# Kernel optimization log

Measured on AMD Instinct MI355X. Metric: run time of the kernel, lower is better.

The kernel has to match this reference:

```python
import jax, jax.numpy as jnp
import numpy as np

N = 100000      # nodes
E = 1600000     # edges (avg degree 16)
D_IN, D_H1, D_H2, D_OUT = 512, 256, 256, 64


def setup_inputs() -> dict:
    key = jax.random.key(0)
    ks = jax.random.split(key, 8)
    x = jax.random.normal(ks[0], (N, D_IN), dtype=jnp.float32)
    row = jax.random.randint(ks[1], (E,), 0, N, dtype=jnp.int32)
    col = jax.random.randint(ks[2], (E,), 0, N, dtype=jnp.int32)
    vals = jax.random.uniform(ks[3], (E,), dtype=jnp.float32)
    # xavier-normal-ish scaling for weights
    W1 = jax.random.normal(ks[4], (D_IN, D_H1), dtype=jnp.float32) * np.sqrt(2.0 / (D_IN + D_H1))
    W2 = jax.random.normal(ks[5], (D_H1, D_H2), dtype=jnp.float32) * np.sqrt(2.0 / (D_H1 + D_H2))
    W3 = jax.random.normal(ks[6], (D_H2, D_OUT), dtype=jnp.float32) * np.sqrt(2.0 / (D_H2 + D_OUT))
    b1 = jnp.zeros((D_H1,), dtype=jnp.float32)
    b2 = jnp.zeros((D_H2,), dtype=jnp.float32)
    b3 = jnp.zeros((D_OUT,), dtype=jnp.float32)
    return {"x": x, "row": row, "col": col, "vals": vals,
            "W1": W1, "b1": b1, "W2": W2, "b2": b2, "W3": W3, "b3": b3}


def reference(x, row, col, vals, W1, b1, W2, b2, W3, b3):
    n = x.shape[0]

    def spmm(h):
        # out[i] = sum_{e: row[e]==i} vals[e] * h[col[e]]  (COO spmm)
        return jax.ops.segment_sum(vals[:, None] * h[col], row, num_segments=n)

    # layer 1: linear -> spmm -> relu  (dropout p=0 -> identity)
    h = jax.nn.relu(spmm(x @ W1 + b1))
    # layer 2
    h = jax.nn.relu(spmm(h @ W2 + b2))
    # output layer: no activation, no dropout
    return spmm(h @ W3 + b3)
```

## Files before the change

### kernel.cpp

```cpp
#include <hip/hip_runtime.h>

typedef _Float16 f16;
typedef _Float16 f16x4 __attribute__((ext_vector_type(4)));
typedef _Float16 f16x8 __attribute__((ext_vector_type(8)));
typedef float f32x4 __attribute__((ext_vector_type(4)));

#define DEVI __device__ __forceinline__

static constexpr int CAP = 64;

DEVI f16x8 cvt8(float4 a, float4 b) {
  f16x8 r;
  r[0] = (f16)a.x; r[1] = (f16)a.y; r[2] = (f16)a.z; r[3] = (f16)a.w;
  r[4] = (f16)b.x; r[5] = (f16)b.y; r[6] = (f16)b.z; r[7] = (f16)b.w;
  return r;
}

__global__ __launch_bounds__(256)
void prep_w(const float* __restrict__ W1, const float* __restrict__ W2,
            const float* __restrict__ W3, f16* __restrict__ WT1,
            f16* __restrict__ WT2, f16* __restrict__ WT3) {
  int t = blockIdx.x * 256 + threadIdx.x;
  const float* W; f16* O; int N; int u;
  if (t < 16384) {
    W = W1; O = WT1; N = 256; u = t;
  } else if (t < 16384 + 8192) {
    W = W2; O = WT2; N = 256; u = t - 16384;
  } else if (t < 16384 + 8192 + 2048) {
    W = W3; O = WT3; N = 64;  u = t - 24576;
  } else return;
  const int per = (N >> 4) * 64;
  const int kc = u / per;
  const int rem = u - kc * per;
  const int l = rem & 63;
  const int n = ((rem >> 6) << 4) + (l & 15);
  const int kb = kc * 32 + ((l >> 4) << 3);
  f16x8 o;
#pragma unroll
  for (int j = 0; j < 8; ++j) o[j] = (f16)W[(size_t)(kb + j) * N + n];
  *(f16x8*)(O + (size_t)u * 8) = o;
}

__global__ __launch_bounds__(256)
void build_slots(const int* __restrict__ row, const int* __restrict__ col,
                 const float* __restrict__ vals, int* __restrict__ cnt,
                 int2* __restrict__ slots, int E) {
  int e = blockIdx.x * 256 + threadIdx.x;
  if (e >= E) return;
  int r = row[e];
  int p = atomicAdd(&cnt[r], 1);
  if (p < CAP) slots[(size_t)r * CAP + p] = make_int2(col[e], __float_as_int(vals[e]));
}

__global__ __launch_bounds__(256, 2)
void gemm_l1_direct(const float* __restrict__ A, const f16* __restrict__ WT,
                    const float* __restrict__ bias, f16* __restrict__ C, int M) {
  constexpr int K = 512, N = 256;
  const int tid = threadIdx.x;
  const int wave = tid >> 6, lane = tid & 63;
  const int wm = wave >> 1, wn = wave & 1;
  const int quad = lane >> 4, l16 = lane & 15;
  const int r0 = blockIdx.x * 64 + wm * 32;

  const float4* ap0 = (const float4*)(A + (size_t)min(r0 + l16, M - 1) * K + quad * 8);
  const float4* ap1 = (const float4*)(A + (size_t)min(r0 + 16 + l16, M - 1) * K + quad * 8);
  const f16x8* bp = (const f16x8*)WT + (size_t)(wn * 8) * 64 + lane;

  f32x4 acc[2][8];
#pragma unroll
  for (int mt = 0; mt < 2; ++mt)
#pragma unroll
    for (int nt = 0; nt < 8; ++nt) {
      f32x4 z = {0.f, 0.f, 0.f, 0.f};
      acc[mt][nt] = z;
    }

  float4 ab[2][2][2];
  f16x8 bb[2][8];

#define L1_LOAD(P, KB)                                   \
  ab[P][0][0] = ap0[(KB) * 8];                           \
  ab[P][0][1] = ap0[(KB) * 8 + 1];                       \
  ab[P][1][0] = ap1[(KB) * 8];                           \
  ab[P][1][1] = ap1[(KB) * 8 + 1];                       \
  {                                                      \
    _Pragma("unroll")                                    \
    for (int nt = 0; nt < 8; ++nt)                       \
      bb[P][nt] = bp[((KB) * 16 + nt) * 64];             \
  }

  L1_LOAD(0, 0)
#pragma unroll
  for (int kb = 0; kb < 16; ++kb) {
    const int cur = kb & 1, nxt = cur ^ 1;
    if (kb + 1 < 16) { L1_LOAD(nxt, kb + 1) }
    f16x8 af0 = cvt8(ab[cur][0][0], ab[cur][0][1]);
    f16x8 af1 = cvt8(ab[cur][1][0], ab[cur][1][1]);
#pragma unroll
    for (int nt = 0; nt < 8; ++nt)
      acc[0][nt] = __builtin_amdgcn_mfma_f32_16x16x32_f16(af0, bb[cur][nt], acc[0][nt], 0, 0, 0);
#pragma unroll
    for (int nt = 0; nt < 8; ++nt)
      acc[1][nt] = __builtin_amdgcn_mfma_f32_16x16x32_f16(af1, bb[cur][nt], acc[1][nt], 0, 0, 0);
  }
#undef L1_LOAD

  float bv[8];
#pragma unroll
  for (int nt = 0; nt < 8; ++nt) bv[nt] = bias[wn * 128 + nt * 16 + l16];
#pragma unroll
  for (int mt = 0; mt < 2; ++mt) {
#pragma unroll
    for (int nt = 0; nt < 8; ++nt) {
      int colg = wn * 128 + nt * 16 + l16;
#pragma unroll
      for (int r = 0; r < 4; ++r) {
        int grow = r0 + mt * 16 + quad * 4 + r;
        if (grow < M)
          C[(size_t)grow * N + colg] = (f16)(acc[mt][nt][r] + bv[nt]);
      }
    }
  }
}

template <int NTILES>
__global__ __launch_bounds__(256, 2)
void gemm_direct(const f16* __restrict__ A, const f16* __restrict__ WT,
                 const float* __restrict__ bias, f16* __restrict__ C, int M) {
  constexpr int K = 256, N = NTILES * 64, NF16 = N / 16;
  const int tid = threadIdx.x;
  const int wave = tid >> 6, lane = tid & 63;
  const int quad = lane >> 4, l16 = lane & 15;
  const int gw = blockIdx.x * 4 + wave;
  const int mtile = (NTILES == 1) ? gw : (gw / NTILES);
  const int ntile = (NTILES == 1) ? 0 : (gw % NTILES);
  const int r0 = mtile * 64;
  if (r0 >= M) return;

  const f16x8* ap0 = (const f16x8*)(A + (size_t)min(r0 + l16, M - 1) * K) + quad;
  const f16x8* ap1 = (const f16x8*)(A + (size_t)min(r0 + 16 + l16, M - 1) * K) + quad;
  const f16x8* ap2 = (const f16x8*)(A + (size_t)min(r0 + 32 + l16, M - 1) * K) + quad;
  const f16x8* ap3 = (const f16x8*)(A + (size_t)min(r0 + 48 + l16, M - 1) * K) + quad;
  const f16x8* bp = (const f16x8*)WT + (size_t)(ntile * 4) * 64 + lane;

  f32x4 acc[4][4];
#pragma unroll
  for (int mt = 0; mt < 4; ++mt)
#pragma unroll
    for (int nt = 0; nt < 4; ++nt) {
      f32x4 z = {0.f, 0.f, 0.f, 0.f};
      acc[mt][nt] = z;
    }

  f16x8 ab[2][4], bb[2][4];

#define GD_LOAD(P, KB)                                   \
  ab[P][0] = ap0[(KB) * 4];                              \
  ab[P][1] = ap1[(KB) * 4];                              \
  ab[P][2] = ap2[(KB) * 4];                              \
  ab[P][3] = ap3[(KB) * 4];                              \
  {                                                      \
    _Pragma("unroll")                                    \
    for (int nt = 0; nt < 4; ++nt)                       \
      bb[P][nt] = bp[((KB) * NF16 + nt) * 64];           \
  }

  GD_LOAD(0, 0)
#pragma unroll
  for (int kb = 0; kb < 8; ++kb) {
    const int cur = kb & 1, nxt = cur ^ 1;
    if (kb + 1 < 8) { GD_LOAD(nxt, kb + 1) }
#pragma unroll
    for (int mt = 0; mt < 4; ++mt)
#pragma unroll
      for (int nt = 0; nt < 4; ++nt)
        acc[mt][nt] = __builtin_amdgcn_mfma_f32_16x16x32_f16(ab[cur][mt], bb[cur][nt], acc[mt][nt], 0, 0, 0);
  }
#undef GD_LOAD

  float bv[4];
#pragma unroll
  for (int nt = 0; nt < 4; ++nt) bv[nt] = bias[ntile * 64 + nt * 16 + l16];
#pragma unroll
  for (int mt = 0; mt < 4; ++mt) {
#pragma unroll
    for (int nt = 0; nt < 4; ++nt) {
      int colg = ntile * 64 + nt * 16 + l16;
#pragma unroll
      for (int r = 0; r < 4; ++r) {
        int grow = r0 + mt * 16 + quad * 4 + r;
        if (grow < M)
          C[(size_t)grow * N + colg] = (f16)(acc[mt][nt][r] + bv[nt]);
      }
    }
  }
}

__global__ __launch_bounds__(256)
void spmm_relu256(const f16* __restrict__ T, const int2* __restrict__ slots,
                  const int* __restrict__ cnt, f16* __restrict__ H, int nrows) {
  const int wave = threadIdx.x >> 6, lane = threadIdx.x & 63;
  const int i = blockIdx.x * 4 + wave;
  if (i >= nrows) return;
  const int c = min(cnt[i], CAP);
  const int2* sl = slots + (size_t)i * CAP;
  float a0 = 0.f, a1 = 0.f, a2 = 0.f, a3 = 0.f;
  int j = 0;
  for (; j + 8 <= c; j += 8) {
    int2 e[8];
#pragma unroll
    for (int q = 0; q < 8; ++q) e[q] = sl[j + q];
    f16x4 u[8];
#pragma unroll
    for (int q = 0; q < 8; ++q)
      u[q] = ((const f16x4*)(T + (size_t)e[q].x * 256))[lane];
#pragma unroll
    for (int q = 0; q < 8; ++q) {
      float v = __int_as_float(e[q].y);
      a0 += v * (float)u[q].x; a1 += v * (float)u[q].y;
      a2 += v * (float)u[q].z; a3 += v * (float)u[q].w;
    }
  }
  for (; j + 2 <= c; j += 2) {
    int2 e0 = sl[j], e1 = sl[j + 1];
    f16x4 u0 = ((const f16x4*)(T + (size_t)e0.x * 256))[lane];
    f16x4 u1 = ((const f16x4*)(T + (size_t)e1.x * 256))[lane];
    float v0 = __int_as_float(e0.y), v1 = __int_as_float(e1.y);
    a0 += v0 * (float)u0.x + v1 * (float)u1.x;
    a1 += v0 * (float)u0.y + v1 * (float)u1.y;
    a2 += v0 * (float)u0.z + v1 * (float)u1.z;
    a3 += v0 * (float)u0.w + v1 * (float)u1.w;
  }
  if (j < c) {
    int2 e = sl[j];
    f16x4 u = ((const f16x4*)(T + (size_t)e.x * 256))[lane];
    float v = __int_as_float(e.y);
    a0 += v * (float)u.x; a1 += v * (float)u.y;
    a2 += v * (float)u.z; a3 += v * (float)u.w;
  }
  f16x4 o;
  o.x = (f16)fmaxf(a0, 0.f); o.y = (f16)fmaxf(a1, 0.f);
  o.z = (f16)fmaxf(a2, 0.f); o.w = (f16)fmaxf(a3, 0.f);
  ((f16x4*)(H + (size_t)i * 256))[lane] = o;
}

__global__ __launch_bounds__(256)
void spmm_out64(const f16* __restrict__ T, const int2* __restrict__ slots,
                const int* __restrict__ cnt, float* __restrict__ out, int nrows) {
  const int wave = threadIdx.x >> 6, lane = threadIdx.x & 63;
  const int i = blockIdx.x * 4 + wave;
  if (i >= nrows) return;
  const int c = min(cnt[i], CAP);
  const int2* sl = slots + (size_t)i * CAP;
  float a = 0.f;
  int j = 0;
  for (; j + 8 <= c; j += 8) {
    int2 e[8];
#pragma unroll
    for (int q = 0; q < 8; ++q) e[q] = sl[j + q];
    float u[8];
#pragma unroll
    for (int q = 0; q < 8; ++q) u[q] = (float)T[(size_t)e[q].x * 64 + lane];
#pragma unroll
    for (int q = 0; q < 8; ++q) a += __int_as_float(e[q].y) * u[q];
  }
  for (; j < c; ++j) {
    int2 e = sl[j];
    a += __int_as_float(e.y) * (float)T[(size_t)e.x * 64 + lane];
  }
  out[(size_t)i * 64 + lane] = a;
}

extern "C" void kernel_launch(void* const* d_in, const int* in_sizes, int n_in,
                              void* d_out, int out_size, void* d_ws, size_t ws_size,
                              hipStream_t stream) {
  const float* x    = (const float*)d_in[0];
  const int*   row  = (const int*)d_in[1];
  const int*   col  = (const int*)d_in[2];
  const float* vals = (const float*)d_in[3];
  const float* W1   = (const float*)d_in[4];
  const float* b1   = (const float*)d_in[5];
  const float* W2   = (const float*)d_in[6];
  const float* b2   = (const float*)d_in[7];
  const float* W3   = (const float*)d_in[8];
  const float* b3   = (const float*)d_in[9];
  float* out = (float*)d_out;

  const int N = in_sizes[0] / 512;
  const int E = in_sizes[1];

  char* ws = (char*)d_ws;
  const size_t MiB = 1ull << 20;
  int*  cnt   = (int*)ws;
  int2* slots = (int2*)(ws + 1 * MiB);
  f16*  WT1   = (f16*)(ws + 52 * MiB);
  f16*  WT2   = WT1 + 256 * 512;
  f16*  WT3   = WT2 + 256 * 256;
  f16*  T     = (f16*)(ws + 53 * MiB);
  f16*  H     = (f16*)(ws + 104 * MiB);

  hipMemsetAsync(cnt, 0, (size_t)N * sizeof(int), stream);
  prep_w<<<(16384 + 8192 + 2048 + 255) / 256, 256, 0, stream>>>(W1, W2, W3, WT1, WT2, WT3);
  build_slots<<<(E + 255) / 256, 256, 0, stream>>>(row, col, vals, cnt, slots, E);

  const int mt64 = (N + 63) / 64;
  dim3 gs((N + 3) / 4);

  gemm_l1_direct<<<mt64, 256, 0, stream>>>(x, WT1, b1, T, N);
  spmm_relu256<<<gs, 256, 0, stream>>>(T, slots, cnt, H, N);
  gemm_direct<4><<<mt64, 256, 0, stream>>>(H, WT2, b2, T, N);
  spmm_relu256<<<gs, 256, 0, stream>>>(T, slots, cnt, H, N);
  gemm_direct<1><<<(mt64 + 3) / 4, 256, 0, stream>>>(H, WT3, b3, T, N);
  spmm_out64<<<gs, 256, 0, stream>>>(T, slots, cnt, out, N);
}
```

Measured before the change: 845.5 us.

## Stage GEMM tiles through LDS with async global-to-LDS triple buffering

After: 836.0 us. No clear change (-1.1%).

```diff
diff --git a/kernel.cpp b/kernel.cpp
--- a/kernel.cpp
+++ b/kernel.cpp
@@ -8,6 +8,16 @@
 #define DEVI __device__ __forceinline__
 
 static constexpr int CAP = 64;
+
+#define WAITVM(N) asm volatile("s_waitcnt vmcnt(" #N ")" ::: "memory")
+#define WAITLGKM0 asm volatile("s_waitcnt lgkmcnt(0)" ::: "memory")
+#define BAR() __builtin_amdgcn_s_barrier()
+
+DEVI void g2l16(const void* g, void* l) {
+  __builtin_amdgcn_global_load_lds(
+      (const __attribute__((address_space(1))) void*)g,
+      (__attribute__((address_space(3))) void*)l, 16, 0, 0);
+}
 
 DEVI f16x8 cvt8(float4 a, float4 b) {
   f16x8 r;
@@ -52,96 +62,23 @@
   if (p < CAP) slots[(size_t)r * CAP + p] = make_int2(col[e], __float_as_int(vals[e]));
 }
 
-__global__ __launch_bounds__(256, 2)
-void gemm_l1_direct(const float* __restrict__ A, const f16* __restrict__ WT,
-                    const float* __restrict__ bias, f16* __restrict__ C, int M) {
-  constexpr int K = 512, N = 256;
+__global__ __launch_bounds__(256)
+void gemm_l1_pipe(const float* __restrict__ A, const f16* __restrict__ WT,
+                  const float* __restrict__ bias, f16* __restrict__ C, int M) {
+  constexpr int NK = 16;
+  __shared__ f16 As[2][128 * 32];
+  __shared__ f16 Bs[3][128 * 32];
+
   const int tid = threadIdx.x;
   const int wave = tid >> 6, lane = tid & 63;
   const int wm = wave >> 1, wn = wave & 1;
   const int quad = lane >> 4, l16 = lane & 15;
-  const int r0 = blockIdx.x * 64 + wm * 32;
-
-  const float4* ap0 = (const float4*)(A + (size_t)min(r0 + l16, M - 1) * K + quad * 8);
-  const float4* ap1 = (const float4*)(A + (size_t)min(r0 + 16 + l16, M - 1) * K + quad * 8);
-  const f16x8* bp = (const f16x8*)WT + (size_t)(wn * 8) * 64 + lane;
-
-  f32x4 acc[2][8];
-#pragma unroll
-  for (int mt = 0; mt < 2; ++mt)
-#pragma unroll
-    for (int nt = 0; nt < 8; ++nt) {
-      f32x4 z = {0.f, 0.f, 0.f, 0.f};
-      acc[mt][nt] = z;
-    }
-
-  float4 ab[2][2][2];
-  f16x8 bb[2][8];
-
-#define L1_LOAD(P, KB)                                   \
-  ab[P][0][0] = ap0[(KB) * 8];                           \
-  ab[P][0][1] = ap0[(KB) * 8 + 1];                       \
-  ab[P][1][0] = ap1[(KB) * 8];                           \
-  ab[P][1][1] = ap1[(KB) * 8 + 1];                       \
-  {                                                      \
-    _Pragma("unroll")                                    \
-    for (int nt = 0; nt < 8; ++nt)                       \
-      bb[P][nt] = bp[((KB) * 16 + nt) * 64];             \
-  }
-
-  L1_LOAD(0, 0)
-#pragma unroll
-  for (int kb = 0; kb < 16; ++kb) {
-    const int cur = kb & 1, nxt = cur ^ 1;
-    if (kb + 1 < 16) { L1_LOAD(nxt, kb + 1) }
-    f16x8 af0 = cvt8(ab[cur][0][0], ab[cur][0][1]);
-    f16x8 af1 = cvt8(ab[cur][1][0], ab[cur][1][1]);
-#pragma unroll
-    for (int nt = 0; nt < 8; ++nt)
-      acc[0][nt] = __builtin_amdgcn_mfma_f32_16x16x32_f16(af0, bb[cur][nt], acc[0][nt], 0, 0, 0);
-#pragma unroll
-    for (int nt = 0; nt < 8; ++nt)
-      acc[1][nt] = __builtin_amdgcn_mfma_f32_16x16x32_f16(af1, bb[cur][nt], acc[1][nt], 0, 0, 0);
-  }
-#undef L1_LOAD
-
-  float bv[8];
-#pragma unroll
-  for (int nt = 0; nt < 8; ++nt) bv[nt] = bias[wn * 128 + nt * 16 + l16];
-#pragma unroll
-  for (int mt = 0; mt < 2; ++mt) {
-#pragma unroll
-    for (int nt = 0; nt < 8; ++nt) {
-      int colg = wn * 128 + nt * 16 + l16;
-#pragma unroll
-      for (int r = 0; r < 4; ++r) {
-        int grow = r0 + mt * 16 + quad * 4 + r;
-        if (grow < M)
-          C[(size_t)grow * N + colg] = (f16)(acc[mt][nt][r] + bv[nt]);
-      }
-    }
-  }
-}
-
-template <int NTILES>
-__global__ __launch_bounds__(256, 2)
-void gemm_direct(const f16* __restrict__ A, const f16* __restrict__ WT,
-                 const float* __restrict__ bias, f16* __restrict__ C, int M) {
-  constexpr int K = 256, N = NTILES * 64, NF16 = N / 16;
-  const int tid = threadIdx.x;
-  const int wave = tid >> 6, lane = tid & 63;
-  const int quad = lane >> 4, l16 = lane & 15;
-  const int gw = blockIdx.x * 4 + wave;
-  const int mtile = (NTILES == 1) ? gw : (gw / NTILES);
-  const int ntile = (NTILES == 1) ? 0 : (gw % NTILES);
-  const int r0 = mtile * 64;
-  if (r0 >= M) return;
-
-  const f16x8* ap0 = (const f16x8*)(A + (size_t)min(r0 + l16, M - 1) * K) + quad;
-  const f16x8* ap1 = (const f16x8*)(A + (size_t)min(r0 + 16 + l16, M - 1) * K) + quad;
-  const f16x8* ap2 = (const f16x8*)(A + (size_t)min(r0 + 32 + l16, M - 1) * K) + quad;
-  const f16x8* ap3 = (const f16x8*)(A + (size_t)min(r0 + 48 + l16, M - 1) * K) + quad;
-  const f16x8* bp = (const f16x8*)WT + (size_t)(ntile * 4) * 64 + lane;
+  const int r0 = blockIdx.x * 128;
+  const int bn = blockIdx.y;
+
+  const float* asrc0 = A + (size_t)min(r0 + (wave * 2 + 0) * 16 + l16, M - 1) * 512 + quad * 8;
+  const float* asrc1 = A + (size_t)min(r0 + (wave * 2 + 1) * 16 + l16, M - 1) * 512 + quad * 8;
+  const f16* bsrc = WT + ((size_t)(bn * 8 + wave * 2)) * 512 + lane * 8;
 
   f32x4 acc[4][4];
 #pragma unroll
@@ -152,45 +89,153 @@
       acc[mt][nt] = z;
     }
 
-  f16x8 ab[2][4], bb[2][4];
-
-#define GD_LOAD(P, KB)                                   \
-  ab[P][0] = ap0[(KB) * 4];                              \
-  ab[P][1] = ap1[(KB) * 4];                              \
-  ab[P][2] = ap2[(KB) * 4];                              \
-  ab[P][3] = ap3[(KB) * 4];                              \
-  {                                                      \
-    _Pragma("unroll")                                    \
-    for (int nt = 0; nt < 4; ++nt)                       \
-      bb[P][nt] = bp[((KB) * NF16 + nt) * 64];           \
-  }
-
-  GD_LOAD(0, 0)
-#pragma unroll
-  for (int kb = 0; kb < 8; ++kb) {
-    const int cur = kb & 1, nxt = cur ^ 1;
-    if (kb + 1 < 8) { GD_LOAD(nxt, kb + 1) }
+  float4 ra[2][2][2];
+
+#define P1_ISSUE(KB, SET, BS)                                          \
+  {                                                                    \
+    const float4* pa0 = (const float4*)(asrc0 + (KB) * 32);            \
+    ra[SET][0][0] = pa0[0]; ra[SET][0][1] = pa0[1];                    \
+    const float4* pa1 = (const float4*)(asrc1 + (KB) * 32);            \
+    ra[SET][1][0] = pa1[0]; ra[SET][1][1] = pa1[1];                    \
+    g2l16(bsrc + (size_t)(KB) * 16 * 512, &Bs[BS][(wave * 2) * 512]);  \
+    g2l16(bsrc + (size_t)(KB) * 16 * 512 + 512,                        \
+          &Bs[BS][(wave * 2 + 1) * 512]);                              \
+  }
+#define P1_CVT(SET, SL)                                                \
+  *(f16x8*)&As[SL][(wave * 2) * 512 + lane * 8] =                      \
+      cvt8(ra[SET][0][0], ra[SET][0][1]);                              \
+  *(f16x8*)&As[SL][(wave * 2 + 1) * 512 + lane * 8] =                  \
+      cvt8(ra[SET][1][0], ra[SET][1][1]);
+
+  P1_ISSUE(0, 0, 0)
+  P1_ISSUE(1, 1, 1)
+  WAITVM(8);
+  P1_CVT(0, 0)
+
+#pragma unroll
+  for (int kb = 0; kb < NK; ++kb) {
+    if (kb < NK - 2) { P1_ISSUE(kb + 2, kb & 1, (kb + 2) % 3) }
+    if (kb < NK - 2) { WAITVM(8); }
+    else if (kb == NK - 2) { WAITVM(2); }
+    else { WAITVM(0); }
+    if (kb < NK - 1) { P1_CVT((kb + 1) & 1, (kb + 1) & 1) }
+    WAITLGKM0;
+    BAR();
+    f16x8 af[4], bf[4];
 #pragma unroll
     for (int mt = 0; mt < 4; ++mt)
+      af[mt] = *(const f16x8*)&As[kb & 1][(wm * 4 + mt) * 512 + lane * 8];
+#pragma unroll
+    for (int nt = 0; nt < 4; ++nt)
+      bf[nt] = *(const f16x8*)&Bs[kb % 3][(wn * 4 + nt) * 512 + lane * 8];
+#pragma unroll
+    for (int mt = 0; mt < 4; ++mt)
 #pragma unroll
       for (int nt = 0; nt < 4; ++nt)
-        acc[mt][nt] = __builtin_amdgcn_mfma_f32_16x16x32_f16(ab[cur][mt], bb[cur][nt], acc[mt][nt], 0, 0, 0);
-  }
-#undef GD_LOAD
+        acc[mt][nt] = __builtin_amdgcn_mfma_f32_16x16x32_f16(af[mt], bf[nt], acc[mt][nt], 0, 0, 0);
+    BAR();
+  }
+#undef P1_ISSUE
+#undef P1_CVT
 
   float bv[4];
 #pragma unroll
-  for (int nt = 0; nt < 4; ++nt) bv[nt] = bias[ntile * 64 + nt * 16 + l16];
+  for (int nt = 0; nt < 4; ++nt) bv[nt] = bias[bn * 128 + wn * 64 + nt * 16 + l16];
 #pragma unroll
   for (int mt = 0; mt < 4; ++mt) {
 #pragma unroll
     for (int nt = 0; nt < 4; ++nt) {
-      int colg = ntile * 64 + nt * 16 + l16;
+      int colg = bn * 128 + wn * 64 + nt * 16 + l16;
 #pragma unroll
       for (int r = 0; r < 4; ++r) {
-        int grow = r0 + mt * 16 + quad * 4 + r;
+        int grow = r0 + wm * 64 + mt * 16 + quad * 4 + r;
         if (grow < M)
-          C[(size_t)grow * N + colg] = (f16)(acc[mt][nt][r] + bv[nt]);
+          C[(size_t)grow * 256 + colg] = (f16)(acc[mt][nt][r] + bv[nt]);
+      }
+    }
+  }
+}
+
+template <int BN, int NTOT>
+__global__ __launch_bounds__(256)
+void gemm_pipe(const f16* __restrict__ A, const f16* __restrict__ WT,
+               const float* __restrict__ bias, f16* __restrict__ C, int M) {
+  constexpr int NT = BN / 32, BFRAGS = BN / 16, NB = BN / 64;
+  constexpr int NF16 = NTOT / 16, NK = 8;
+  __shared__ f16 As[3][128 * 32];
+  __shared__ f16 Bs[3][BN * 32];
+
+  const int tid = threadIdx.x;
+  const int wave = tid >> 6, lane = tid & 63;
+  const int wm = wave >> 1, wn = wave & 1;
+  const int quad = lane >> 4, l16 = lane & 15;
+  const int r0 = blockIdx.x * 128;
+  const int bn = blockIdx.y;
+
+  const f16* asrc0 = A + (size_t)min(r0 + (wave * 2 + 0) * 16 + l16, M - 1) * 256 + quad * 8;
+  const f16* asrc1 = A + (size_t)min(r0 + (wave * 2 + 1) * 16 + l16, M - 1) * 256 + quad * 8;
+  const f16* bsrc = WT + (size_t)(bn * BFRAGS + wave * NB) * 512 + lane * 8;
+
+  f32x4 acc[4][NT];
+#pragma unroll
+  for (int mt = 0; mt < 4; ++mt)
+#pragma unroll
+    for (int nt = 0; nt < NT; ++nt) {
+      f32x4 z = {0.f, 0.f, 0.f, 0.f};
+      acc[mt][nt] = z;
+    }
+
+#define P2_ISSUE(KB, SL)                                               \
+  {                                                                    \
+    g2l16(asrc0 + (KB) * 32, &As[SL][(wave * 2) * 512]);               \
+    g2l16(asrc1 + (KB) * 32, &As[SL][(wave * 2 + 1) * 512]);           \
+    _Pragma("unroll")                                                  \
+    for (int t = 0; t < NB; ++t)                                       \
+      g2l16(bsrc + ((size_t)(KB) * NF16 + t) * 512,                    \
+            &Bs[SL][(wave * NB + t) * 512]);                           \
+  }
+
+  P2_ISSUE(0, 0)
+  P2_ISSUE(1, 1)
+
+#pragma unroll
+  for (int kb = 0; kb < NK; ++kb) {
+    if (kb < NK - 2) { P2_ISSUE(kb + 2, (kb + 2) % 3) }
+    if (kb < NK - 2) {
+      if constexpr (BN == 128) { WAITVM(8); } else { WAITVM(6); }
+    } else if (kb == NK - 2) {
+      if constexpr (BN == 128) { WAITVM(4); } else { WAITVM(3); }
+    } else { WAITVM(0); }
+    BAR();
+    f16x8 af[4], bf[NT];
+#pragma unroll
+    for (int mt = 0; mt < 4; ++mt)
+      af[mt] = *(const f16x8*)&As[kb % 3][(wm * 4 + mt) * 512 + lane * 8];
+#pragma unroll
+    for (int nt = 0; nt < NT; ++nt)
+      bf[nt] = *(const f16x8*)&Bs[kb % 3][(wn * NT + nt) * 512 + lane * 8];
+#pragma unroll
+    for (int mt = 0; mt < 4; ++mt)
+#pragma unroll
+      for (int nt = 0; nt < NT; ++nt)
+        acc[mt][nt] = __builtin_amdgcn_mfma_f32_16x16x32_f16(af[mt], bf[nt], acc[mt][nt], 0, 0, 0);
+    BAR();
+  }
+#undef P2_ISSUE
+
+  float bv[NT];
+#pragma unroll
+  for (int nt = 0; nt < NT; ++nt) bv[nt] = bias[bn * BN + wn * (BN / 2) + nt * 16 + l16];
+#pragma unroll
+  for (int mt = 0; mt < 4; ++mt) {
+#pragma unroll
+    for (int nt = 0; nt < NT; ++nt) {
+      int colg = bn * BN + wn * (BN / 2) + nt * 16 + l16;
+#pragma unroll
+      for (int r = 0; r < 4; ++r) {
+        int grow = r0 + wm * 64 + mt * 16 + quad * 4 + r;
+        if (grow < M)
+          C[(size_t)grow * NTOT + colg] = (f16)(acc[mt][nt][r] + bv[nt]);
       }
     }
   }
@@ -303,13 +348,13 @@
   prep_w<<<(16384 + 8192 + 2048 + 255) / 256, 256, 0, stream>>>(W1, W2, W3, WT1, WT2, WT3);
   build_slots<<<(E + 255) / 256, 256, 0, stream>>>(row, col, vals, cnt, slots, E);
 
-  const int mt64 = (N + 63) / 64;
+  const int mt128 = (N + 127) / 128;
   dim3 gs((N + 3) / 4);
 
-  gemm_l1_direct<<<mt64, 256, 0, stream>>>(x, WT1, b1, T, N);
+  gemm_l1_pipe<<<dim3(mt128, 2), 256, 0, stream>>>(x, WT1, b1, T, N);
   spmm_relu256<<<gs, 256, 0, stream>>>(T, slots, cnt, H, N);
-  gemm_direct<4><<<mt64, 256, 0, stream>>>(H, WT2, b2, T, N);
+  gemm_pipe<128, 256><<<dim3(mt128, 2), 256, 0, stream>>>(H, WT2, b2, T, N);
   spmm_relu256<<<gs, 256, 0, stream>>>(T, slots, cnt, H, N);
-  gemm_direct<1><<<(mt64 + 3) / 4, 256, 0, stream>>>(H, WT3, b3, T, N);
+  gemm_pipe<64, 64><<<dim3(mt128, 1), 256, 0, stream>>>(H, WT3, b3, T, N);
   spmm_out64<<<gs, 256, 0, stream>>>(T, slots, cnt, out, N);
 }
```
